# Optimization experiments

Measured on AMD Instinct MI355X. Metric: run time of the kernel, lower is better.

Reference implementation:

```python
import jax, jax.numpy as jnp
import numpy as np

B, N, K, DIM = 2, 20000, 16, 256


def _mlp(x, W, b):
    # torch nn.Linear: x @ W.T + b, then LeakyReLU(0.1)
    return jax.nn.leaky_relu(x @ W.T + b, negative_slope=0.1)


def _lfa(features, geom, idx, W, b):
    # features: [B, N, C]; geom: [B, N, K, 4]; idx: [B, N, K]
    t = _mlp(geom, W, b)                                  # [B, N, K, d_lfa]
    fn = jax.vmap(lambda f, i: f[i])(features, idx)       # gather neighbors: [B, N, K, C]
    # mean over K of concat == concat of means (faithful, avoids big concat)
    return jnp.concatenate([t.mean(axis=2), fn.mean(axis=2)], axis=-1)


def _linear_init(key, out_f, in_f):
    k1, k2 = jax.random.split(key)
    bound = 1.0 / np.sqrt(in_f)
    W = jax.random.uniform(k1, (out_f, in_f), jnp.float32, -bound, bound)
    b = jax.random.uniform(k2, (out_f,), jnp.float32, -bound, bound)
    return W, b


def setup_inputs() -> dict:
    key = jax.random.key(0)
    ks = jax.random.split(key, 8)
    W_init, b_init = _linear_init(ks[0], DIM // 4, DIM)
    W_l1, b_l1 = _linear_init(ks[1], DIM // 4, 4)
    W_l2, b_l2 = _linear_init(ks[2], DIM // 2, 4)
    W_fin, b_fin = _linear_init(ks[3], DIM, DIM)
    W_id, b_id = _linear_init(ks[4], DIM, DIM)
    return {
        "input_tensor": jax.random.normal(ks[5], (B, N, DIM), jnp.float32),
        "geometric_features": jax.random.normal(ks[6], (B, N, K, 4), jnp.float32),
        "neighbor_indices": jax.random.randint(ks[7], (B, N, K), 0, N, jnp.int64 if jax.config.jax_enable_x64 else jnp.int32),
        "W_init": W_init, "b_init": b_init,
        "W_l1": W_l1, "b_l1": b_l1,
        "W_l2": W_l2, "b_l2": b_l2,
        "W_fin": W_fin, "b_fin": b_fin,
        "W_id": W_id, "b_id": b_id,
    }


def reference(input_tensor, geometric_features, neighbor_indices,
              W_init, b_init, W_l1, b_l1, W_l2, b_l2,
              W_fin, b_fin, W_id, b_id):
    residual = input_tensor
    x = _mlp(input_tensor, W_init, b_init)                       # [B, N, dim/4]
    x = _lfa(x, geometric_features, neighbor_indices, W_l1, b_l1)  # [B, N, dim/2]
    x = _lfa(x, geometric_features, neighbor_indices, W_l2, b_l2)  # [B, N, dim]
    x = _mlp(x, W_fin, b_fin)
    return x + _mlp(residual, W_id, b_id)
```

## Files before the change

### kernel.cpp

```cpp
#include <hip/hip_runtime.h>
#include <hip/hip_bf16.h>

#define BN   40000
#define NPTS 20000
#define KNN  16
#define DIM  256

typedef __attribute__((ext_vector_type(8))) short bf16x8;
typedef __attribute__((ext_vector_type(4))) float f32x4;
typedef __attribute__((ext_vector_type(16))) float f32x16;

__device__ __forceinline__ float lrelu(float v) { return fmaxf(v, 0.1f * v); }
__device__ __forceinline__ float bs2f(short s) {
    union { unsigned u; float f; } c; c.u = ((unsigned)(unsigned short)s) << 16;
    return c.f;
}
__device__ __forceinline__ short f2bs(float f) {
    __hip_bfloat16 h = __float2bfloat16(f);
    return *reinterpret_cast<short*>(&h);
}
__device__ __forceinline__ bf16x8 ldf32_bf16x8(const float* p) {
    const float4 a = ((const float4*)p)[0];
    const float4 b = ((const float4*)p)[1];
    bf16x8 r;
    r[0]=f2bs(a.x); r[1]=f2bs(a.y); r[2]=f2bs(a.z); r[3]=f2bs(a.w);
    r[4]=f2bs(b.x); r[5]=f2bs(b.y); r[6]=f2bs(b.z); r[7]=f2bs(b.w);
    return r;
}

__device__ __forceinline__ void dma16(const void* g, void* l) {
    __builtin_amdgcn_global_load_lds(
        (const __attribute__((address_space(1))) unsigned int*)g,
        (__attribute__((address_space(3))) unsigned int*)l, 16, 0, 0);
}

__global__ void __launch_bounds__(256) prep_kernel(
    const int* __restrict__ idxw, int* __restrict__ flag,
    const float* __restrict__ Wf, const float* __restrict__ Wi,
    const float* __restrict__ Wn,
    short* __restrict__ Wt, short* __restrict__ Wnt)
{
    if (blockIdx.x == 0) {
        __shared__ int red[256];
        int t = threadIdx.x;
        int v = 0;
#pragma unroll
        for (int it = 0; it < 64; ++it)
            v |= idxw[2 * (t + it * 256) + 1];
        red[t] = v;
        __syncthreads();
        for (int s = 128; s > 0; s >>= 1) {
            if (t < s) red[t] |= red[t + s];
            __syncthreads();
        }
        if (t == 0) *flag = (red[0] != 0) ? 1 : 0;
        return;
    }
    int t = (blockIdx.x - 1) * 256 + threadIdx.x;
    if (t < 32768) {
        int mat = (t >> 14) & 1;
        int tt  = t & 16383;
        float4 v = mat ? ((const float4*)Wi)[tt] : ((const float4*)Wf)[tt];
        int n  = tt >> 6;
        int k  = (tt & 63) * 4;
        int kk = k >> 5, q = (k >> 3) & 3, j = k & 7;
        short4 o; o.x=f2bs(v.x); o.y=f2bs(v.y); o.z=f2bs(v.z); o.w=f2bs(v.w);
        *(short4*)(Wt + ((size_t)((kk*2 + mat)*4 + q))*2048 + n*8 + j) = o;
    } else {
        int tt = t - 32768;
        float4 v = ((const float4*)Wn)[tt];
        int n  = tt >> 6;
        int k  = (tt & 63) * 4;
        int kk = k >> 5, q = (k >> 3) & 3, j = k & 7;
        short4 o; o.x=f2bs(v.x); o.y=f2bs(v.y); o.z=f2bs(v.z); o.w=f2bs(v.w);
        *(short4*)(Wnt + ((size_t)((kk*4 + q)*64 + n))*8 + j) = o;
    }
}

__global__ void __launch_bounds__(256) stage2_kernel(
    const float* __restrict__ geom,
    const float* __restrict__ W1, const float* __restrict__ B1,
    const float* __restrict__ W2, const float* __restrict__ B2,
    const float* __restrict__ X,
    const short* __restrict__ Wnt,
    const float* __restrict__ b_init,
    __hip_bfloat16* __restrict__ x2,
    __hip_bfloat16* __restrict__ x3,
    __hip_bfloat16* __restrict__ x1)
{
    __shared__ short wbuf[16384];

    if (blockIdx.x >= 625) {
        int bid = blockIdx.x - 625;
        int t = threadIdx.x;
        int wave = t >> 6, lane = t & 63;
        int r = lane & 15, q = lane >> 4;
        {
            const char* W8 = (const char*)Wnt;
            char* L8 = (char*)wbuf;
#pragma unroll
            for (int rd = 0; rd < 8; ++rd) {
                int off = (wave * 8 + rd) * 1024 + lane * 16;
                dma16(W8 + off, L8 + off);
            }
        }
        int m0 = bid * 64 + wave * 16;
        const float* Xs = X + (size_t)(m0 + r) * DIM + q * 8;
        bf16x8 a[8];
#pragma unroll
        for (int kk = 0; kk < 8; ++kk) a[kk] = ldf32_bf16x8(Xs + kk * 32);
        __syncthreads();

        f32x4 acc[4];
#pragma unroll
        for (int nt = 0; nt < 4; ++nt) acc[nt] = (f32x4){0.f,0.f,0.f,0.f};
#pragma unroll
        for (int kk = 0; kk < 8; ++kk) {
#pragma unroll
            for (int nt = 0; nt < 4; ++nt) {
                bf16x8 b = *(const bf16x8*)&wbuf[((kk*4 + q)*64 + nt*16 + r) * 8];
                acc[nt] = __builtin_amdgcn_mfma_f32_16x16x32_bf16(a[kk], b, acc[nt], 0, 0, 0);
            }
        }
#pragma unroll
        for (int nt = 0; nt < 4; ++nt) {
            int col = nt * 16 + r;
            float bvx = b_init[col];
#pragma unroll
            for (int i = 0; i < 4; ++i) {
                float v = lrelu(acc[nt][i] + bvx);
                x1[(size_t)(m0 + q*4 + i) * 64 + col] = __float2bfloat16(v);
            }
        }
        return;
    }

    const int lane = threadIdx.x & 63;
    const int wv   = threadIdx.x >> 6;
    const int c31  = lane & 31;
    const int hi   = lane >> 5;
    const int wglob = blockIdx.x * 4 + wv;

    bf16x8 bfr[6]; float bv[6];
#pragma unroll
    for (int tt = 0; tt < 6; ++tt) {
        bfr[tt] = (bf16x8){0,0,0,0,0,0,0,0};
        const float* Wrow;
        if (tt < 2) { Wrow = W1 + (size_t)(tt*32 + c31) * 4;     bv[tt] = B1[tt*32 + c31]; }
        else        { Wrow = W2 + (size_t)((tt-2)*32 + c31) * 4; bv[tt] = B2[(tt-2)*32 + c31]; }
        if (hi == 0) {
            const float4 w4 = *(const float4*)Wrow;
            bfr[tt][0]=f2bs(w4.x); bfr[tt][1]=f2bs(w4.y);
            bfr[tt][2]=f2bs(w4.z); bfr[tt][3]=f2bs(w4.w);
        }
    }
    f32x16 ZR;
#pragma unroll
    for (int i = 0; i < 16; ++i) ZR[i] = 0.f;

    float4 g = (float4){0.f,0.f,0.f,0.f};
    if (hi == 0)
        g = *(const float4*)(geom +
            ((size_t)((wglob * 8) * 2 + (c31 >> 4)) * KNN + (c31 & 15)) * 4);

#pragma unroll
    for (int it = 0; it < 8; ++it) {
        const int p0 = (wglob * 8 + it) * 2;
        const float4 gc = g;
        if (it < 7 && hi == 0)
            g = *(const float4*)(geom +
                ((size_t)(p0 + 2 + (c31 >> 4)) * KNN + (c31 & 15)) * 4);

        bf16x8 a = (bf16x8){0,0,0,0,0,0,0,0};
        if (hi == 0) { a[0]=f2bs(gc.x); a[1]=f2bs(gc.y); a[2]=f2bs(gc.z); a[3]=f2bs(gc.w); }

        f32x16 acc[6];
#pragma unroll
        for (int tt = 0; tt < 6; ++tt)
            acc[tt] = __builtin_amdgcn_mfma_f32_32x32x16_bf16(a, bfr[tt], ZR, 0, 0, 0);

#pragma unroll
        for (int tt = 0; tt < 6; ++tt) {
            float sA = 0.f, sB = 0.f;
#pragma unroll
            for (int i = 0; i < 8; ++i)  sA += lrelu(acc[tt][i]     + bv[tt]);
#pragma unroll
            for (int i = 0; i < 8; ++i)  sB += lrelu(acc[tt][i + 8] + bv[tt]);
            sA += __shfl_xor(sA, 32, 64);
            sB += __shfl_xor(sB, 32, 64);
            const float s = (hi ? sB : sA) * (1.f / 16.f);
            const short v = f2bs(s);
            if (tt < 2) ((short*)x2)[(size_t)(p0 + hi) * 128 + tt*32 + c31] = v;
            else        ((short*)x3)[(size_t)(p0 + hi) * 256 + (tt-2)*32 + c31] = v;
        }
    }
}

__global__ void __launch_bounds__(256) gather1_kernel(
    const int* __restrict__ idxw, const int* __restrict__ flag,
    const __hip_bfloat16* __restrict__ x1,
    __hip_bfloat16* __restrict__ x2)
{
    int t = blockIdx.x * 256 + threadIdx.x;
    int p = t >> 3, j = t & 7;
    int lane = threadIdx.x & 63;
    int dual = (*flag == 0) ? 2 : 1;
    int base = (p >= NPTS) ? NPTS : 0;
    int i0 = idxw[((size_t)p * 16 + 2*j)     * dual];
    int i1 = idxw[((size_t)p * 16 + 2*j + 1) * dual];
    int g8 = lane & 56;
    float acc[8];
#pragma unroll
    for (int i = 0; i < 8; ++i) acc[i] = 0.f;
#pragma unroll
    for (int k = 0; k < 8; ++k) {
        int rA = base + __shfl(i0, g8 + k, 64);
        int rB = base + __shfl(i1, g8 + k, 64);
        bf16x8 vA = *(const bf16x8*)((const short*)x1 + (size_t)rA * 64 + j * 8);
        bf16x8 vB = *(const bf16x8*)((const short*)x1 + (size_t)rB * 64 + j * 8);
#pragma unroll
        for (int i = 0; i < 8; ++i) acc[i] += bs2f(vA[i]) + bs2f(vB[i]);
    }
    bf16x8 o;
#pragma unroll
    for (int i = 0; i < 8; ++i) o[i] = f2bs(acc[i] * (1.f/16.f));
    *(bf16x8*)((short*)x2 + (size_t)p * 128 + 64 + j * 8) = o;
}

__global__ void __launch_bounds__(256) gather2_kernel(
    const int* __restrict__ idxw, const int* __restrict__ flag,
    const __hip_bfloat16* __restrict__ x2,
    __hip_bfloat16* __restrict__ x3)
{
    int t = blockIdx.x * 256 + threadIdx.x;
    int p = t >> 4, j = t & 15;
    int lane = threadIdx.x & 63;
    int dual = (*flag == 0) ? 2 : 1;
    int base = (p >= NPTS) ? NPTS : 0;
    int myi = idxw[((size_t)p * 16 + j) * dual];
    int g16 = lane & 48;
    float acc[8];
#pragma unroll
    for (int i = 0; i < 8; ++i) acc[i] = 0.f;
#pragma unroll
    for (int k = 0; k < KNN; ++k) {
        int row = base + __shfl(myi, g16 + k, 64);
        bf16x8 v = *(const bf16x8*)((const short*)x2 + (size_t)row * 128 + j * 8);
#pragma unroll
        for (int i = 0; i < 8; ++i) acc[i] += bs2f(v[i]);
    }
    bf16x8 o;
#pragma unroll
    for (int i = 0; i < 8; ++i) o[i] = f2bs(acc[i] * (1.f/16.f));
    *(bf16x8*)((short*)x3 + (size_t)p * 256 + 128 + j * 8) = o;
}

__global__ void __launch_bounds__(512, 2) final_mfma(
    const __hip_bfloat16* __restrict__ X3,
    const float* __restrict__ RES,
    const short* __restrict__ Wt,
    const float* __restrict__ Bf,
    const float* __restrict__ Bi,
    float* __restrict__ OUT)
{
    __shared__ short lw[65536];
    const int t    = threadIdx.x;
    const int wave = t >> 6, lane = t & 63;
    const int r = lane & 15, q = lane >> 4;
    const int rg = wave >> 1, cg = wave & 1;
    const int ch = blockIdx.x & 1;
    const int p0 = (blockIdx.x >> 1) * 320;

    {
        const char* WtB = (const char*)Wt;
        char* L = (char*)lw;
#pragma unroll
        for (int i = 0; i < 16; ++i) {
            int c = wave * 8 + (i >> 1);
            int d = i & 1;
            int mat = c >> 5, kk = (c >> 2) & 7, qq = c & 3;
            int src_sh = ((kk * 2 + mat) * 4 + qq) * 2048 + ch * 1024;
            dma16(WtB + (size_t)src_sh * 2 + d * 1024 + lane * 16,
                  L + (c * 2 + d) * 1024 + lane * 16);
        }
    }
    const int cb = ch * 128 + cg * 64;
    float bfv[4], biv[4];
#pragma unroll
    for (int nt = 0; nt < 4; ++nt) {
        bfv[nt] = Bf[cb + nt * 16 + r];
        biv[nt] = Bi[cb + nt * 16 + r];
    }
    __syncthreads();

    const short* bpf = lw + q * 1024 + (cg * 64 + r) * 8;
    const short* bpi = bpf + 32768;

#pragma unroll
    for (int tt = 0; tt < 5; ++tt) {
        const int row = p0 + tt * 64 + rg * 16 + r;
        const short* x3r = (const short*)X3 + (size_t)row * DIM + q * 8;
        const float* rsr = RES + (size_t)row * DIM + q * 8;

        bf16x8 a1[8];
        float4 rw[16];
#pragma unroll
        for (int kk = 0; kk < 8; ++kk) {
            rw[2*kk]   = ((const float4*)rsr)[kk * 8];
            rw[2*kk+1] = ((const float4*)rsr)[kk * 8 + 1];
            a1[kk] = *(const bf16x8*)(x3r + kk * 32);
        }

        f32x4 acc1[4], acc2[4];
#pragma unroll
        for (int nt = 0; nt < 4; ++nt) {
            acc1[nt] = (f32x4){0.f,0.f,0.f,0.f};
            acc2[nt] = (f32x4){0.f,0.f,0.f,0.f};
        }
#pragma unroll
        for (int kk = 0; kk < 8; ++kk) {
            bf16x8 a2;
            {
                const float4 lo = rw[2*kk], hi = rw[2*kk+1];
                a2[0]=f2bs(lo.x); a2[1]=f2bs(lo.y); a2[2]=f2bs(lo.z); a2[3]=f2bs(lo.w);
                a2[4]=f2bs(hi.x); a2[5]=f2bs(hi.y); a2[6]=f2bs(hi.z); a2[7]=f2bs(hi.w);
            }
#pragma unroll
            for (int nt = 0; nt < 4; ++nt) {
                bf16x8 b1 = *(const bf16x8*)(bpf + kk * 4096 + nt * 128);
                bf16x8 b2 = *(const bf16x8*)(bpi + kk * 4096 + nt * 128);
                acc1[nt] = __builtin_amdgcn_mfma_f32_16x16x32_bf16(a1[kk], b1, acc1[nt], 0, 0, 0);
                acc2[nt] = __builtin_amdgcn_mfma_f32_16x16x32_bf16(a2,    b2, acc2[nt], 0, 0, 0);
            }
        }
#pragma unroll
        for (int nt = 0; nt < 4; ++nt) {
            const int col = cb + nt * 16 + r;
#pragma unroll
            for (int i = 0; i < 4; ++i) {
                float v = lrelu(acc1[nt][i] + bfv[nt]) + lrelu(acc2[nt][i] + biv[nt]);
                OUT[(size_t)(p0 + tt * 64 + rg * 16 + q * 4 + i) * DIM + col] = v;
            }
        }
    }
}

extern "C" void kernel_launch(void* const* d_in, const int* in_sizes, int n_in,
                              void* d_out, int out_size, void* d_ws, size_t ws_size,
                              hipStream_t stream)
{
    const float* input  = (const float*)d_in[0];
    const float* geom   = (const float*)d_in[1];
    const int*   idxw   = (const int*)d_in[2];
    const float* W_init = (const float*)d_in[3];
    const float* b_init = (const float*)d_in[4];
    const float* W_l1   = (const float*)d_in[5];
    const float* b_l1   = (const float*)d_in[6];
    const float* W_l2   = (const float*)d_in[7];
    const float* b_l2   = (const float*)d_in[8];
    const float* W_fin  = (const float*)d_in[9];
    const float* b_fin  = (const float*)d_in[10];
    const float* W_id   = (const float*)d_in[11];
    const float* b_id   = (const float*)d_in[12];
    float* out = (float*)d_out;

    char* ws = (char*)d_ws;
    int* flag = (int*)ws;
    short* Wt  = (short*)(ws + 16);
    short* Wnt = (short*)(ws + 16 + 262144);
    __hip_bfloat16* x2 = (__hip_bfloat16*)(ws + 16 + 5120000);
    __hip_bfloat16* x3 = (__hip_bfloat16*)(ws + 16 + 15360000);
    __hip_bfloat16* x1 = (__hip_bfloat16*)d_out;

    prep_kernel<<<145, 256, 0, stream>>>(idxw, flag, W_fin, W_id, W_init,
                                         Wt, Wnt);
    stage2_kernel<<<1250, 256, 0, stream>>>(geom, W_l1, b_l1, W_l2, b_l2,
                                            input, Wnt, b_init, x2, x3, x1);
    gather1_kernel<<<1250, 256, 0, stream>>>(idxw, flag, x1, x2);
    gather2_kernel<<<2500, 256, 0, stream>>>(idxw, flag, x2, x3);
    final_mfma<<<250, 512, 0, stream>>>(x3, input, Wt, b_fin, b_id, out);
}
```

Measured before the change: 195.8 us.

## Fold prep work into stage2, convert W_init in-block, pair batches in gathers

Removes the separate prep kernel by adding extra blocks to stage2 that compute the index-width flag and transpose and convert W_fin/W_id. Each init-MLP block now converts W_init fp32 to bf16 straight into LDS instead of DMA-ing a pre-converted copy, and batches its X loads. The gather kernels now handle both batch halves per thread, halving their grids and doubling the loads in flight per thread. The cost is redundant W_init conversion in every init block and higher register pressure in the gathers.

```diff
diff --git a/kernel.cpp b/kernel.cpp
--- a/kernel.cpp
+++ b/kernel.cpp
@@ -34,30 +34,40 @@
         (__attribute__((address_space(3))) unsigned int*)l, 16, 0, 0);
 }
 
-__global__ void __launch_bounds__(256) prep_kernel(
-    const int* __restrict__ idxw, int* __restrict__ flag,
+__global__ void __launch_bounds__(256) stage2_kernel(
+    const float* __restrict__ geom,
+    const float* __restrict__ W1, const float* __restrict__ B1,
+    const float* __restrict__ W2, const float* __restrict__ B2,
+    const float* __restrict__ X,
+    const float* __restrict__ Wn,
+    const float* __restrict__ b_init,
+    const int* __restrict__ idxw,
     const float* __restrict__ Wf, const float* __restrict__ Wi,
-    const float* __restrict__ Wn,
-    short* __restrict__ Wt, short* __restrict__ Wnt)
+    short* __restrict__ Wt, int* __restrict__ flag,
+    __hip_bfloat16* __restrict__ x2,
+    __hip_bfloat16* __restrict__ x3,
+    __hip_bfloat16* __restrict__ x1)
 {
-    if (blockIdx.x == 0) {
-        __shared__ int red[256];
-        int t = threadIdx.x;
-        int v = 0;
-#pragma unroll
-        for (int it = 0; it < 64; ++it)
-            v |= idxw[2 * (t + it * 256) + 1];
-        red[t] = v;
-        __syncthreads();
-        for (int s = 128; s > 0; s >>= 1) {
-            if (t < s) red[t] |= red[t + s];
+    __shared__ short wbuf[16384];
+
+    if (blockIdx.x >= 1250) {
+        if (blockIdx.x == 1378) {
+            __shared__ int red[256];
+            int t = threadIdx.x;
+            int v = 0;
+#pragma unroll
+            for (int it = 0; it < 64; ++it)
+                v |= idxw[2 * (t + it * 256) + 1];
+            red[t] = v;
             __syncthreads();
-        }
-        if (t == 0) *flag = (red[0] != 0) ? 1 : 0;
-        return;
-    }
-    int t = (blockIdx.x - 1) * 256 + threadIdx.x;
-    if (t < 32768) {
+            for (int s = 128; s > 0; s >>= 1) {
+                if (t < s) red[t] |= red[t + s];
+                __syncthreads();
+            }
+            if (t == 0) *flag = (red[0] != 0) ? 1 : 0;
+            return;
+        }
+        int t = (blockIdx.x - 1250) * 256 + threadIdx.x;
         int mat = (t >> 14) & 1;
         int tt  = t & 16383;
         float4 v = mat ? ((const float4*)Wi)[tt] : ((const float4*)Wf)[tt];
@@ -66,29 +76,8 @@
         int kk = k >> 5, q = (k >> 3) & 3, j = k & 7;
         short4 o; o.x=f2bs(v.x); o.y=f2bs(v.y); o.z=f2bs(v.z); o.w=f2bs(v.w);
         *(short4*)(Wt + ((size_t)((kk*2 + mat)*4 + q))*2048 + n*8 + j) = o;
-    } else {
-        int tt = t - 32768;
-        float4 v = ((const float4*)Wn)[tt];
-        int n  = tt >> 6;
-        int k  = (tt & 63) * 4;
-        int kk = k >> 5, q = (k >> 3) & 3, j = k & 7;
-        short4 o; o.x=f2bs(v.x); o.y=f2bs(v.y); o.z=f2bs(v.z); o.w=f2bs(v.w);
-        *(short4*)(Wnt + ((size_t)((kk*4 + q)*64 + n))*8 + j) = o;
-    }
-}
-
-__global__ void __launch_bounds__(256) stage2_kernel(
-    const float* __restrict__ geom,
-    const float* __restrict__ W1, const float* __restrict__ B1,
-    const float* __restrict__ W2, const float* __restrict__ B2,
-    const float* __restrict__ X,
-    const short* __restrict__ Wnt,
-    const float* __restrict__ b_init,
-    __hip_bfloat16* __restrict__ x2,
-    __hip_bfloat16* __restrict__ x3,
-    __hip_bfloat16* __restrict__ x1)
-{
-    __shared__ short wbuf[16384];
+        return;
+    }
 
     if (blockIdx.x >= 625) {
         int bid = blockIdx.x - 625;
@@ -96,19 +85,38 @@
         int wave = t >> 6, lane = t & 63;
         int r = lane & 15, q = lane >> 4;
         {
-            const char* W8 = (const char*)Wnt;
-            char* L8 = (char*)wbuf;
-#pragma unroll
-            for (int rd = 0; rd < 8; ++rd) {
-                int off = (wave * 8 + rd) * 1024 + lane * 16;
-                dma16(W8 + off, L8 + off);
+            const float4* Wn4 = (const float4*)Wn;
+#pragma unroll
+            for (int i = 0; i < 16; ++i) {
+                int tt = t * 16 + i;
+                float4 v = Wn4[tt];
+                int n  = tt >> 6;
+                int k  = (tt & 63) * 4;
+                int kk = k >> 5, qq = (k >> 3) & 3, j = k & 7;
+                short4 o; o.x=f2bs(v.x); o.y=f2bs(v.y); o.z=f2bs(v.z); o.w=f2bs(v.w);
+                *(short4*)&wbuf[((kk*4 + qq)*64 + n)*8 + j] = o;
             }
         }
         int m0 = bid * 64 + wave * 16;
-        const float* Xs = X + (size_t)(m0 + r) * DIM + q * 8;
+        const float4* X4 = (const float4*)(X + (size_t)(m0 + r) * DIM + q * 8);
         bf16x8 a[8];
 #pragma unroll
-        for (int kk = 0; kk < 8; ++kk) a[kk] = ldf32_bf16x8(Xs + kk * 32);
+        for (int g = 0; g < 2; ++g) {
+            float4 rwm[8];
+#pragma unroll
+            for (int kk = 0; kk < 4; ++kk) {
+                rwm[2*kk]   = X4[(g*4 + kk) * 8];
+                rwm[2*kk+1] = X4[(g*4 + kk) * 8 + 1];
+            }
+#pragma unroll
+            for (int kk = 0; kk < 4; ++kk) {
+                const float4 lo = rwm[2*kk], hi2 = rwm[2*kk+1];
+                bf16x8 av;
+                av[0]=f2bs(lo.x);  av[1]=f2bs(lo.y);  av[2]=f2bs(lo.z);  av[3]=f2bs(lo.w);
+                av[4]=f2bs(hi2.x); av[5]=f2bs(hi2.y); av[6]=f2bs(hi2.z); av[7]=f2bs(hi2.w);
+                a[g*4 + kk] = av;
+            }
+        }
         __syncthreads();
 
         f32x4 acc[4];
@@ -205,26 +213,38 @@
     int p = t >> 3, j = t & 7;
     int lane = threadIdx.x & 63;
     int dual = (*flag == 0) ? 2 : 1;
-    int base = (p >= NPTS) ? NPTS : 0;
-    int i0 = idxw[((size_t)p * 16 + 2*j)     * dual];
-    int i1 = idxw[((size_t)p * 16 + 2*j + 1) * dual];
     int g8 = lane & 56;
-    float acc[8];
-#pragma unroll
-    for (int i = 0; i < 8; ++i) acc[i] = 0.f;
+    int iA0 = idxw[((size_t)p * 16 + 2*j)     * dual];
+    int iA1 = idxw[((size_t)p * 16 + 2*j + 1) * dual];
+    int iB0 = idxw[((size_t)(p + NPTS) * 16 + 2*j)     * dual];
+    int iB1 = idxw[((size_t)(p + NPTS) * 16 + 2*j + 1) * dual];
+    float aA[8], aB[8];
+#pragma unroll
+    for (int i = 0; i < 8; ++i) { aA[i] = 0.f; aB[i] = 0.f; }
 #pragma unroll
     for (int k = 0; k < 8; ++k) {
-        int rA = base + __shfl(i0, g8 + k, 64);
-        int rB = base + __shfl(i1, g8 + k, 64);
-        bf16x8 vA = *(const bf16x8*)((const short*)x1 + (size_t)rA * 64 + j * 8);
-        bf16x8 vB = *(const bf16x8*)((const short*)x1 + (size_t)rB * 64 + j * 8);
-#pragma unroll
-        for (int i = 0; i < 8; ++i) acc[i] += bs2f(vA[i]) + bs2f(vB[i]);
-    }
-    bf16x8 o;
-#pragma unroll
-    for (int i = 0; i < 8; ++i) o[i] = f2bs(acc[i] * (1.f/16.f));
-    *(bf16x8*)((short*)x2 + (size_t)p * 128 + 64 + j * 8) = o;
+        int rA0 = __shfl(iA0, g8 + k, 64);
+        int rA1 = __shfl(iA1, g8 + k, 64);
+        int rB0 = NPTS + __shfl(iB0, g8 + k, 64);
+        int rB1 = NPTS + __shfl(iB1, g8 + k, 64);
+        bf16x8 vA0 = *(const bf16x8*)((const short*)x1 + (size_t)rA0 * 64 + j * 8);
+        bf16x8 vA1 = *(const bf16x8*)((const short*)x1 + (size_t)rA1 * 64 + j * 8);
+        bf16x8 vB0 = *(const bf16x8*)((const short*)x1 + (size_t)rB0 * 64 + j * 8);
+        bf16x8 vB1 = *(const bf16x8*)((const short*)x1 + (size_t)rB1 * 64 + j * 8);
+#pragma unroll
+        for (int i = 0; i < 8; ++i) {
+            aA[i] += bs2f(vA0[i]) + bs2f(vA1[i]);
+            aB[i] += bs2f(vB0[i]) + bs2f(vB1[i]);
+        }
+    }
+    bf16x8 oA, oB;
+#pragma unroll
+    for (int i = 0; i < 8; ++i) {
+        oA[i] = f2bs(aA[i] * (1.f/16.f));
+        oB[i] = f2bs(aB[i] * (1.f/16.f));
+    }
+    *(bf16x8*)((short*)x2 + (size_t)p * 128 + 64 + j * 8) = oA;
+    *(bf16x8*)((short*)x2 + (size_t)(p + NPTS) * 128 + 64 + j * 8) = oB;
 }
 
 __global__ void __launch_bounds__(256) gather2_kernel(
@@ -236,23 +256,32 @@
     int p = t >> 4, j = t & 15;
     int lane = threadIdx.x & 63;
     int dual = (*flag == 0) ? 2 : 1;
-    int base = (p >= NPTS) ? NPTS : 0;
-    int myi = idxw[((size_t)p * 16 + j) * dual];
     int g16 = lane & 48;
-    float acc[8];
-#pragma unroll
-    for (int i = 0; i < 8; ++i) acc[i] = 0.f;
+    int iA = idxw[((size_t)p * 16 + j) * dual];
+    int iB = idxw[((size_t)(p + NPTS) * 16 + j) * dual];
+    float aA[8], aB[8];
+#pragma unroll
+    for (int i = 0; i < 8; ++i) { aA[i] = 0.f; aB[i] = 0.f; }
 #pragma unroll
     for (int k = 0; k < KNN; ++k) {
-        int row = base + __shfl(myi, g16 + k, 64);
-        bf16x8 v = *(const bf16x8*)((const short*)x2 + (size_t)row * 128 + j * 8);
-#pragma unroll
-        for (int i = 0; i < 8; ++i) acc[i] += bs2f(v[i]);
-    }
-    bf16x8 o;
-#pragma unroll
-    for (int i = 0; i < 8; ++i) o[i] = f2bs(acc[i] * (1.f/16.f));
-    *(bf16x8*)((short*)x3 + (size_t)p * 256 + 128 + j * 8) = o;
+        int rA = __shfl(iA, g16 + k, 64);
+        int rB = NPTS + __shfl(iB, g16 + k, 64);
+        bf16x8 vA = *(const bf16x8*)((const short*)x2 + (size_t)rA * 128 + j * 8);
+        bf16x8 vB = *(const bf16x8*)((const short*)x2 + (size_t)rB * 128 + j * 8);
+#pragma unroll
+        for (int i = 0; i < 8; ++i) {
+            aA[i] += bs2f(vA[i]);
+            aB[i] += bs2f(vB[i]);
+        }
+    }
+    bf16x8 oA, oB;
+#pragma unroll
+    for (int i = 0; i < 8; ++i) {
+        oA[i] = f2bs(aA[i] * (1.f/16.f));
+        oB[i] = f2bs(aB[i] * (1.f/16.f));
+    }
+    *(bf16x8*)((short*)x3 + (size_t)p * 256 + 128 + j * 8) = oA;
+    *(bf16x8*)((short*)x3 + (size_t)(p + NPTS) * 256 + 128 + j * 8) = oB;
 }
 
 __global__ void __launch_bounds__(512, 2) final_mfma(
@@ -321,9 +350,9 @@
         for (int kk = 0; kk < 8; ++kk) {
             bf16x8 a2;
             {
-                const float4 lo = rw[2*kk], hi = rw[2*kk+1];
-                a2[0]=f2bs(lo.x); a2[1]=f2bs(lo.y); a2[2]=f2bs(lo.z); a2[3]=f2bs(lo.w);
-                a2[4]=f2bs(hi.x); a2[5]=f2bs(hi.y); a2[6]=f2bs(hi.z); a2[7]=f2bs(hi.w);
+                const float4 lo = rw[2*kk], hi2 = rw[2*kk+1];
+                a2[0]=f2bs(lo.x);  a2[1]=f2bs(lo.y);  a2[2]=f2bs(lo.z);  a2[3]=f2bs(lo.w);
+                a2[4]=f2bs(hi2.x); a2[5]=f2bs(hi2.y); a2[6]=f2bs(hi2.z); a2[7]=f2bs(hi2.w);
             }
 #pragma unroll
             for (int nt = 0; nt < 4; ++nt) {
@@ -367,16 +396,15 @@
     char* ws = (char*)d_ws;
     int* flag = (int*)ws;
     short* Wt  = (short*)(ws + 16);
-    short* Wnt = (short*)(ws + 16 + 262144);
     __hip_bfloat16* x2 = (__hip_bfloat16*)(ws + 16 + 5120000);
     __hip_bfloat16* x3 = (__hip_bfloat16*)(ws + 16 + 15360000);
     __hip_bfloat16* x1 = (__hip_bfloat16*)d_out;
 
-    prep_kernel<<<145, 256, 0, stream>>>(idxw, flag, W_fin, W_id, W_init,
-                                         Wt, Wnt);
-    stage2_kernel<<<1250, 256, 0, stream>>>(geom, W_l1, b_l1, W_l2, b_l2,
-                                            input, Wnt, b_init, x2, x3, x1);
-    gather1_kernel<<<1250, 256, 0, stream>>>(idxw, flag, x1, x2);
-    gather2_kernel<<<2500, 256, 0, stream>>>(idxw, flag, x2, x3);
+    stage2_kernel<<<1379, 256, 0, stream>>>(geom, W_l1, b_l1, W_l2, b_l2,
+                                            input, W_init, b_init,
+                                            idxw, W_fin, W_id, Wt, flag,
+                                            x2, x3, x1);
+    gather1_kernel<<<625, 256, 0, stream>>>(idxw, flag, x1, x2);
+    gather2_kernel<<<1250, 256, 0, stream>>>(idxw, flag, x2, x3);
     final_mfma<<<250, 512, 0, stream>>>(x3, input, Wt, b_fin, b_id, out);
 }
```

Measured after the change: 204.8 us. 4.6% more time.
